# Kernel optimization log

Hardware: AMD Instinct MI355X
Metric: run time of the kernel (lower is better)

The kernel has to match this reference:

```python
import jax, jax.numpy as jnp
import numpy as np

N_NODES = 100000


def gcn_conv(x, W, b, src, dst, num_nodes):
    # PyG GCNConv: h = x @ W; out_i = sum_j norm_ij * h_j + b
    # with self-loops already appended to (src, dst) and
    # norm_ij = deg^{-1/2}[src] * deg^{-1/2}[dst].
    h = x @ W  # [N, out]
    deg = jax.ops.segment_sum(jnp.ones_like(src, dtype=h.dtype), dst, num_segments=num_nodes)
    dinv = jnp.where(deg > 0, jax.lax.rsqrt(deg), 0.0)
    norm = dinv[src] * dinv[dst]  # [E]
    msg = h[src] * norm[:, None]  # [E, out]  (gather + scale)
    out = jax.ops.segment_sum(msg, dst, num_segments=num_nodes)  # scatter-add
    return out + b


def setup_inputs() -> dict:
    key = jax.random.key(0)
    ks = jax.random.split(key, 8)
    x = jax.random.normal(ks[0], (N_NODES, 3), dtype=jnp.float32)
    edge_index = jax.random.randint(ks[1], (2, 3200000), 0, N_NODES, dtype=jnp.int64)

    def glorot(k, fan_in, fan_out):
        s = jnp.sqrt(6.0 / (fan_in + fan_out))
        return jax.random.uniform(k, (fan_in, fan_out), jnp.float32, -s, s)

    W1 = glorot(ks[2], 3, 16)
    b1 = jnp.zeros((16,), jnp.float32)
    W2 = glorot(ks[3], 16, 32)
    b2 = jnp.zeros((32,), jnp.float32)
    W3 = glorot(ks[4], 32, 2)
    b3 = jnp.zeros((2,), jnp.float32)
    return {"x": x, "edge_index": edge_index, "W1": W1, "b1": b1,
            "W2": W2, "b2": b2, "W3": W3, "b3": b3}


def reference(x, edge_index, W1, b1, W2, b2, W3, b3):
    num_nodes = x.shape[0]
    # add self-loops once (GCNConv default add_self_loops=True)
    loops = jnp.arange(num_nodes, dtype=edge_index.dtype)
    src = jnp.concatenate([edge_index[0], loops])
    dst = jnp.concatenate([edge_index[1], loops])

    h = jax.nn.relu(gcn_conv(x, W1, b1, src, dst, num_nodes))
    h = jax.nn.relu(gcn_conv(h, W2, b2, src, dst, num_nodes))
    return gcn_conv(h, W3, b3, src, dst, num_nodes)
```

## Files before the change

kernel.cpp:

```cpp
#include <hip/hip_runtime.h>

static constexpr int NND = 100000;
static constexpr int NED = 3200000;
static constexpr int NB  = (NND + 255) / 256;
static constexpr int NCHUNK = 256;
static constexpr int EPC = NED / NCHUNK;
static constexpr int SCAN_N = NB * NCHUNK;

typedef int int4n __attribute__((ext_vector_type(4)));
typedef _Float16 half4n __attribute__((ext_vector_type(4)));
typedef _Float16 half8n __attribute__((ext_vector_type(8)));


__global__ void k_hist(const int* __restrict__ dst, int* __restrict__ counts) {
    __shared__ int h[NB];
    for (int i = threadIdx.x; i < NB; i += 256) h[i] = 0;
    __syncthreads();
    int c = blockIdx.x;
    const int4n* d4 = reinterpret_cast<const int4n*>(dst + c * EPC);
    for (int i = threadIdx.x; i < EPC / 4; i += 256) {
        int4n v = d4[i];
        atomicAdd(&h[v.x >> 8], 1);
        atomicAdd(&h[v.y >> 8], 1);
        atomicAdd(&h[v.z >> 8], 1);
        atomicAdd(&h[v.w >> 8], 1);
    }
    __syncthreads();
    for (int b = threadIdx.x; b < NB; b += 256)
        counts[b * NCHUNK + c] = h[b];
}


__global__ void k_scan1(const int* __restrict__ in, int* __restrict__ excl,
                        int* __restrict__ blockSums, int n) {
    __shared__ int lds[256];
    int tid = threadIdx.x;
    int base = blockIdx.x * 1024 + tid * 4;
    int v[4]; int sum = 0;
#pragma unroll
    for (int k = 0; k < 4; ++k) { int idx = base + k; v[k] = (idx < n) ? in[idx] : 0; sum += v[k]; }
    lds[tid] = sum; __syncthreads();
    for (int off = 1; off < 256; off <<= 1) {
        int x = lds[tid];
        int y = (tid >= off) ? lds[tid - off] : 0;
        __syncthreads();
        lds[tid] = x + y;
        __syncthreads();
    }
    int run = lds[tid] - sum;
#pragma unroll
    for (int k = 0; k < 4; ++k) { int idx = base + k; if (idx < n) excl[idx] = run; run += v[k]; }
    if (tid == 0) blockSums[blockIdx.x] = lds[255];
}

__global__ void k_scan2(int* __restrict__ blockSums, int nb) {
    __shared__ int lds[128];
    int tid = threadIdx.x;
    int v = (tid < nb) ? blockSums[tid] : 0;
    lds[tid] = v; __syncthreads();
    for (int off = 1; off < 128; off <<= 1) {
        int x = lds[tid];
        int y = (tid >= off) ? lds[tid - off] : 0;
        __syncthreads();
        lds[tid] = x + y;
        __syncthreads();
    }
    if (tid < nb) blockSums[tid] = lds[tid] - v;
}

__global__ void k_scan3(int* __restrict__ excl, const int* __restrict__ blockSums,
                        int n, int e) {
    int i = blockIdx.x * blockDim.x + threadIdx.x;
    if (i < n) excl[i] += blockSums[i >> 10];
    if (i == n) excl[n] = e;
}


__global__ void k_part(const int* __restrict__ src, const int* __restrict__ dst,
                       const int* __restrict__ excl, int* __restrict__ tmp) {
    __shared__ int cur[NB];
    int c = blockIdx.x;
    for (int b = threadIdx.x; b < NB; b += 256) cur[b] = excl[b * NCHUNK + c];
    __syncthreads();
    const int4n* s4 = reinterpret_cast<const int4n*>(src + c * EPC);
    const int4n* d4 = reinterpret_cast<const int4n*>(dst + c * EPC);
    for (int i = threadIdx.x; i < EPC / 4; i += 256) {
        int4n sv = __builtin_nontemporal_load(&s4[i]);
        int4n dv = __builtin_nontemporal_load(&d4[i]);
        int ss[4] = {sv.x, sv.y, sv.z, sv.w};
        int dd[4] = {dv.x, dv.y, dv.z, dv.w};
#pragma unroll
        for (int k = 0; k < 4; ++k) {
            int b = dd[k] >> 8;
            int pos = atomicAdd(&cur[b], 1);
            tmp[pos] = ss[k] | ((dd[k] & 255) << 20);
        }
    }
}


__global__ void k_bucket(const int* __restrict__ excl, const int* __restrict__ tmp,
                         int* __restrict__ ssrc, int* __restrict__ rowptr,
                         float* __restrict__ dinv, const float* __restrict__ x,
                         float4* __restrict__ t4) {
    __shared__ int cnt[256];
    __shared__ int lds[256];
    int b = blockIdx.x, t = threadIdx.x;
    int start = excl[b * NCHUNK];
    int end   = excl[(b + 1) * NCHUNK];
    cnt[t] = 0;
    __syncthreads();
    for (int i = start + t; i < end; i += 256)
        atomicAdd(&cnt[tmp[i] >> 20], 1);
    __syncthreads();
    int v = cnt[t];
    lds[t] = v; __syncthreads();
    for (int off = 1; off < 256; off <<= 1) {
        int xv = lds[t];
        int y = (t >= off) ? lds[t - off] : 0;
        __syncthreads();
        lds[t] = xv + y;
        __syncthreads();
    }
    int node = b * 256 + t;
    int rp = start + lds[t] - v;
    if (node < NND) {
        rowptr[node] = rp;
        float d = rsqrtf((float)(v + 1));
        dinv[node] = d;
        const float* xr = x + (size_t)node * 3;
        t4[node] = make_float4(xr[0] * d, xr[1] * d, xr[2] * d, 0.f);
    }
    if (b == 0 && t == 0) rowptr[NND] = NED;
    cnt[t] = rp;
    __syncthreads();
    for (int i = start + t; i < end; i += 256) {
        int p = tmp[i];
        int pos = atomicAdd(&cnt[p >> 20], 1);
        ssrc[pos] = p & 0xFFFFF;
    }
}


__global__ void k_g4mm1(const int* __restrict__ rowptr, const int* __restrict__ ssrc,
                        const float4* __restrict__ t4, const float* __restrict__ dinv,
                        const float* __restrict__ W1, const float* __restrict__ b1,
                        _Float16* __restrict__ t16, int n) {
    __shared__ float sW[48];
    __shared__ float sb[16];
    if (threadIdx.x < 48) sW[threadIdx.x] = W1[threadIdx.x];
    if (threadIdx.x < 16) sb[threadIdx.x] = b1[threadIdx.x];
    __syncthreads();
    int node = blockIdx.x * blockDim.x + threadIdx.x;
    if (node >= n) return;

    float4 a = t4[node];
    float a0 = a.x, a1 = a.y, a2 = a.z;
    int beg = rowptr[node], end = rowptr[node + 1];
    constexpr int U = 8;
    int j = beg;
    for (; j + U <= end; j += U) {
        int s[U];
#pragma unroll
        for (int k = 0; k < U; ++k) s[k] = ssrc[j + k];
        float4 v[U];
#pragma unroll
        for (int k = 0; k < U; ++k) v[k] = t4[s[k]];
#pragma unroll
        for (int k = 0; k < U; ++k) { a0 += v[k].x; a1 += v[k].y; a2 += v[k].z; }
    }
    for (; j < end; ++j) {
        float4 v = t4[ssrc[j]];
        a0 += v.x; a1 += v.y; a2 += v.z;
    }
    float d = dinv[node];
    float p0 = a0 * d, p1 = a1 * d, p2 = a2 * d;
    _Float16* orow = t16 + (size_t)node * 16;
#pragma unroll
    for (int q = 0; q < 2; ++q) {
        half8n o;
#pragma unroll
        for (int r = 0; r < 8; ++r) {
            int jj = q * 8 + r;
            float h = fmaf(p0, sW[jj], fmaf(p1, sW[16 + jj], fmaf(p2, sW[32 + jj], sb[jj])));
            o[r] = (_Float16)(fmaxf(h, 0.f) * d);
        }
        *reinterpret_cast<half8n*>(orow + q * 8) = o;
    }
}


__global__ void k_g16mm(const int* __restrict__ rowptr, const int* __restrict__ ssrc,
                        const _Float16* __restrict__ t16, const float* __restrict__ dinv,
                        const float* __restrict__ W2, const float* __restrict__ b2,
                        const float* __restrict__ W3, float2* __restrict__ t3, int n) {
    __shared__ float sW2[512];
    __shared__ float sb2[32];
    __shared__ float sW3[64];
    for (int i = threadIdx.x; i < 512; i += 256) sW2[i] = W2[i];
    if (threadIdx.x < 32) sb2[threadIdx.x] = b2[threadIdx.x];
    if (threadIdx.x < 64) sW3[threadIdx.x] = W3[threadIdx.x];
    __syncthreads();

    constexpr int U = 8;
    int i = blockIdx.x * blockDim.x + threadIdx.x;
    int node = i >> 2;
    int fv = i & 3;
    if (node >= n) return;
    int f0 = fv * 4;

    float acc0, acc1, acc2, acc3;
    {
        half4n v = *reinterpret_cast<const half4n*>(t16 + (size_t)node * 16 + f0);
        acc0 = (float)v.x; acc1 = (float)v.y; acc2 = (float)v.z; acc3 = (float)v.w;
    }
    int beg = rowptr[node], end = rowptr[node + 1];
    int j = beg;
    for (; j + U <= end; j += U) {
        int s[U];
#pragma unroll
        for (int k = 0; k < U; ++k) s[k] = ssrc[j + k];
        half4n v[U];
#pragma unroll
        for (int k = 0; k < U; ++k)
            v[k] = *reinterpret_cast<const half4n*>(t16 + (size_t)s[k] * 16 + f0);
#pragma unroll
        for (int k = 0; k < U; ++k) {
            acc0 += (float)v[k].x; acc1 += (float)v[k].y;
            acc2 += (float)v[k].z; acc3 += (float)v[k].w;
        }
    }
    for (; j < end; ++j) {
        half4n v = *reinterpret_cast<const half4n*>(t16 + (size_t)ssrc[j] * 16 + f0);
        acc0 += (float)v.x; acc1 += (float)v.y; acc2 += (float)v.z; acc3 += (float)v.w;
    }
    float d = dinv[node];
    float q[4] = {acc0 * d, acc1 * d, acc2 * d, acc3 * d};

    float p1[4], p2[4], p3[4];
#pragma unroll
    for (int c = 0; c < 4; ++c) p1[c] = __shfl_xor(q[c], 1);
#pragma unroll
    for (int c = 0; c < 4; ++c) { p2[c] = __shfl_xor(q[c], 2); p3[c] = __shfl_xor(p1[c], 2); }

    float uu[16];
#pragma unroll
    for (int c = 0; c < 4; ++c) {
        uu[0 + c]  = fv == 0 ? q[c] : fv == 1 ? p1[c] : fv == 2 ? p2[c] : p3[c];
        uu[4 + c]  = fv == 1 ? q[c] : fv == 0 ? p1[c] : fv == 3 ? p2[c] : p3[c];
        uu[8 + c]  = fv == 2 ? q[c] : fv == 3 ? p1[c] : fv == 0 ? p2[c] : p3[c];
        uu[12 + c] = fv == 3 ? q[c] : fv == 2 ? p1[c] : fv == 1 ? p2[c] : p3[c];
    }

    float t30 = 0.f, t31 = 0.f;
    int jbase = fv * 8;
#pragma unroll
    for (int r = 0; r < 8; ++r) {
        int jj = jbase + r;
        float h = sb2[jj];
#pragma unroll
        for (int k = 0; k < 16; ++k) h = fmaf(uu[k], sW2[k * 32 + jj], h);
        h = fmaxf(h, 0.f);
        t30 = fmaf(h, sW3[jj * 2 + 0], t30);
        t31 = fmaf(h, sW3[jj * 2 + 1], t31);
    }
    t30 += __shfl_xor(t30, 1); t30 += __shfl_xor(t30, 2);
    t31 += __shfl_xor(t31, 1); t31 += __shfl_xor(t31, 2);
    if (fv == 0) t3[node] = make_float2(t30 * d, t31 * d);
}


__global__ void k_g2(const int* __restrict__ rowptr, const int* __restrict__ ssrc,
                     const float2* __restrict__ t3, const float* __restrict__ dinv,
                     const float* __restrict__ b3, float2* __restrict__ out, int n) {
    constexpr int U = 8;
    int node = blockIdx.x * blockDim.x + threadIdx.x;
    if (node >= n) return;
    float2 t = t3[node];
    float a0 = t.x, a1 = t.y;
    int beg = rowptr[node], end = rowptr[node + 1];
    int j = beg;
    for (; j + U <= end; j += U) {
        int s[U];
#pragma unroll
        for (int k = 0; k < U; ++k) s[k] = ssrc[j + k];
        float2 v[U];
#pragma unroll
        for (int k = 0; k < U; ++k) v[k] = t3[s[k]];
#pragma unroll
        for (int k = 0; k < U; ++k) { a0 += v[k].x; a1 += v[k].y; }
    }
    for (; j < end; ++j) {
        float2 v = t3[ssrc[j]];
        a0 += v.x; a1 += v.y;
    }
    float d = dinv[node];
    out[node] = make_float2(fmaf(d, a0, b3[0]), fmaf(d, a1, b3[1]));
}


static inline size_t align256(size_t x) { return (x + 255) & ~(size_t)255; }

extern "C" void kernel_launch(void* const* d_in, const int* in_sizes, int n_in,
                              void* d_out, int out_size, void* d_ws, size_t ws_size,
                              hipStream_t stream) {
    const float* x  = (const float*)d_in[0];
    const int*   ei = (const int*)d_in[1];
    const float* W1 = (const float*)d_in[2];
    const float* b1 = (const float*)d_in[3];
    const float* W2 = (const float*)d_in[4];
    const float* b2 = (const float*)d_in[5];
    const float* W3 = (const float*)d_in[6];
    const float* b3 = (const float*)d_in[7];
    float2* out = (float2*)d_out;

    const int* src = ei;
    const int* dst = ei + NED;

    char* p = (char*)d_ws;
    float* dinv   = (float*)p; p += align256(sizeof(float) * (size_t)NND);
    int*   rowptr = (int*)p;   p += align256(sizeof(int) * (size_t)(NND + 1));
    int*   excl   = (int*)p;   p += align256(sizeof(int) * (size_t)(SCAN_N + 1));
    int*   bsums  = (int*)p;   p += align256(sizeof(int) * 128);
    int*   ssrc   = (int*)p;   p += align256(sizeof(int) * (size_t)NED);
    float4* t4    = (float4*)p; p += align256(sizeof(float4) * (size_t)NND);
    float2* t3    = (float2*)p; p += align256(sizeof(float2) * (size_t)NND);
    char*  q      = p;         p += align256(sizeof(int) * (size_t)NED);
    int*   tmp    = (int*)q;
    _Float16* t16 = (_Float16*)q;

    const int B = 256;
    const int gridN = (NND + B - 1) / B;
    const int grid4N = (NND * 4 + B - 1) / B;
    const int nScanBlocks = (SCAN_N + 1023) / 1024;

    k_hist<<<NCHUNK, B, 0, stream>>>(dst, excl);
    k_scan1<<<nScanBlocks, 256, 0, stream>>>(excl, excl, bsums, SCAN_N);
    k_scan2<<<1, 128, 0, stream>>>(bsums, nScanBlocks);
    k_scan3<<<(SCAN_N + 1 + B - 1) / B, B, 0, stream>>>(excl, bsums, SCAN_N, NED);
    k_part<<<NCHUNK, B, 0, stream>>>(src, dst, excl, tmp);
    k_bucket<<<NB, B, 0, stream>>>(excl, tmp, ssrc, rowptr, dinv, x, t4);

    k_g4mm1<<<gridN, B, 0, stream>>>(rowptr, ssrc, t4, dinv, W1, b1, t16, NND);

    k_g16mm<<<grid4N, B, 0, stream>>>(rowptr, ssrc, t16, dinv, W2, b2, W3, t3, NND);

    k_g2<<<gridN, B, 0, stream>>>(rowptr, ssrc, t3, dinv, b3, out, NND);
}
```

Before: 153.3 us.

## Fold scan fixup into consumers, store layer-1 features in fp16, two lanes per node

Removes the k_scan3 kernel: k_part and k_bucket now add the block-sum offsets themselves when reading the exclusive scan, and the final bucket end is fixed to the edge count. The scaled input features t4 are stored as half4 instead of float4, halving the bytes fetched per edge in the first aggregation. The layer-2 kernel assigns two lanes per node with 8-wide fp16 loads instead of four lanes with 4-wide loads, cutting shuffle work and thread count at the cost of more registers per thread. The fp16 input storage adds some rounding error.

```diff
diff --git a/kernel.cpp b/kernel.cpp
--- a/kernel.cpp
+++ b/kernel.cpp
@@ -68,19 +68,16 @@
     if (tid < nb) blockSums[tid] = lds[tid] - v;
 }
 
-__global__ void k_scan3(int* __restrict__ excl, const int* __restrict__ blockSums,
-                        int n, int e) {
-    int i = blockIdx.x * blockDim.x + threadIdx.x;
-    if (i < n) excl[i] += blockSums[i >> 10];
-    if (i == n) excl[n] = e;
-}
-
 
 __global__ void k_part(const int* __restrict__ src, const int* __restrict__ dst,
-                       const int* __restrict__ excl, int* __restrict__ tmp) {
+                       const int* __restrict__ excl, const int* __restrict__ bsums,
+                       int* __restrict__ tmp) {
     __shared__ int cur[NB];
     int c = blockIdx.x;
-    for (int b = threadIdx.x; b < NB; b += 256) cur[b] = excl[b * NCHUNK + c];
+    for (int b = threadIdx.x; b < NB; b += 256) {
+        int i = b * NCHUNK + c;
+        cur[b] = excl[i] + bsums[i >> 10];
+    }
     __syncthreads();
     const int4n* s4 = reinterpret_cast<const int4n*>(src + c * EPC);
     const int4n* d4 = reinterpret_cast<const int4n*>(dst + c * EPC);
@@ -99,15 +96,19 @@
 }
 
 
-__global__ void k_bucket(const int* __restrict__ excl, const int* __restrict__ tmp,
+__global__ void k_bucket(const int* __restrict__ excl, const int* __restrict__ bsums,
+                         const int* __restrict__ tmp,
                          int* __restrict__ ssrc, int* __restrict__ rowptr,
                          float* __restrict__ dinv, const float* __restrict__ x,
-                         float4* __restrict__ t4) {
+                         half4n* __restrict__ t4) {
     __shared__ int cnt[256];
     __shared__ int lds[256];
     int b = blockIdx.x, t = threadIdx.x;
-    int start = excl[b * NCHUNK];
-    int end   = excl[(b + 1) * NCHUNK];
+    int i0 = b * NCHUNK;
+    int start = excl[i0] + bsums[i0 >> 10];
+    int end;
+    if (b == NB - 1) end = NED;
+    else { int i1 = (b + 1) * NCHUNK; end = excl[i1] + bsums[i1 >> 10]; }
     cnt[t] = 0;
     __syncthreads();
     for (int i = start + t; i < end; i += 256)
@@ -129,7 +130,10 @@
         float d = rsqrtf((float)(v + 1));
         dinv[node] = d;
         const float* xr = x + (size_t)node * 3;
-        t4[node] = make_float4(xr[0] * d, xr[1] * d, xr[2] * d, 0.f);
+        half4n o;
+        o.x = (_Float16)(xr[0] * d); o.y = (_Float16)(xr[1] * d);
+        o.z = (_Float16)(xr[2] * d); o.w = (_Float16)0.f;
+        t4[node] = o;
     }
     if (b == 0 && t == 0) rowptr[NND] = NED;
     cnt[t] = rp;
@@ -143,7 +147,7 @@
 
 
 __global__ void k_g4mm1(const int* __restrict__ rowptr, const int* __restrict__ ssrc,
-                        const float4* __restrict__ t4, const float* __restrict__ dinv,
+                        const half4n* __restrict__ t4, const float* __restrict__ dinv,
                         const float* __restrict__ W1, const float* __restrict__ b1,
                         _Float16* __restrict__ t16, int n) {
     __shared__ float sW[48];
@@ -154,8 +158,11 @@
     int node = blockIdx.x * blockDim.x + threadIdx.x;
     if (node >= n) return;
 
-    float4 a = t4[node];
-    float a0 = a.x, a1 = a.y, a2 = a.z;
+    float a0, a1, a2;
+    {
+        half4n a = t4[node];
+        a0 = (float)a.x; a1 = (float)a.y; a2 = (float)a.z;
+    }
     int beg = rowptr[node], end = rowptr[node + 1];
     constexpr int U = 8;
     int j = beg;
@@ -163,15 +170,17 @@
         int s[U];
 #pragma unroll
         for (int k = 0; k < U; ++k) s[k] = ssrc[j + k];
-        float4 v[U];
+        half4n v[U];
 #pragma unroll
         for (int k = 0; k < U; ++k) v[k] = t4[s[k]];
 #pragma unroll
-        for (int k = 0; k < U; ++k) { a0 += v[k].x; a1 += v[k].y; a2 += v[k].z; }
+        for (int k = 0; k < U; ++k) {
+            a0 += (float)v[k].x; a1 += (float)v[k].y; a2 += (float)v[k].z;
+        }
     }
     for (; j < end; ++j) {
-        float4 v = t4[ssrc[j]];
-        a0 += v.x; a1 += v.y; a2 += v.z;
+        half4n v = t4[ssrc[j]];
+        a0 += (float)v.x; a1 += (float)v.y; a2 += (float)v.z;
     }
     float d = dinv[node];
     float p0 = a0 * d, p1 = a1 * d, p2 = a2 * d;
@@ -204,15 +213,16 @@
 
     constexpr int U = 8;
     int i = blockIdx.x * blockDim.x + threadIdx.x;
-    int node = i >> 2;
-    int fv = i & 3;
+    int node = i >> 1;
+    int half = i & 1;
     if (node >= n) return;
-    int f0 = fv * 4;
-
-    float acc0, acc1, acc2, acc3;
+    int f0 = half * 8;
+
+    float acc[8];
     {
-        half4n v = *reinterpret_cast<const half4n*>(t16 + (size_t)node * 16 + f0);
-        acc0 = (float)v.x; acc1 = (float)v.y; acc2 = (float)v.z; acc3 = (float)v.w;
+        half8n v = *reinterpret_cast<const half8n*>(t16 + (size_t)node * 16 + f0);
+#pragma unroll
+        for (int c = 0; c < 8; ++c) acc[c] = (float)v[c];
     }
     int beg = rowptr[node], end = rowptr[node + 1];
     int j = beg;
@@ -220,42 +230,41 @@
         int s[U];
 #pragma unroll
         for (int k = 0; k < U; ++k) s[k] = ssrc[j + k];
-        half4n v[U];
+        half8n v[U];
 #pragma unroll
         for (int k = 0; k < U; ++k)
-            v[k] = *reinterpret_cast<const half4n*>(t16 + (size_t)s[k] * 16 + f0);
+            v[k] = *reinterpret_cast<const half8n*>(t16 + (size_t)s[k] * 16 + f0);
 #pragma unroll
         for (int k = 0; k < U; ++k) {
-            acc0 += (float)v[k].x; acc1 += (float)v[k].y;
-            acc2 += (float)v[k].z; acc3 += (float)v[k].w;
+#pragma unroll
+            for (int c = 0; c < 8; ++c) acc[c] += (float)v[k][c];
         }
     }
     for (; j < end; ++j) {
-        half4n v = *reinterpret_cast<const half4n*>(t16 + (size_t)ssrc[j] * 16 + f0);
-        acc0 += (float)v.x; acc1 += (float)v.y; acc2 += (float)v.z; acc3 += (float)v.w;
+        half8n v = *reinterpret_cast<const half8n*>(t16 + (size_t)ssrc[j] * 16 + f0);
+#pragma unroll
+        for (int c = 0; c < 8; ++c) acc[c] += (float)v[c];
     }
     float d = dinv[node];
-    float q[4] = {acc0 * d, acc1 * d, acc2 * d, acc3 * d};
-
-    float p1[4], p2[4], p3[4];
-#pragma unroll
-    for (int c = 0; c < 4; ++c) p1[c] = __shfl_xor(q[c], 1);
-#pragma unroll
-    for (int c = 0; c < 4; ++c) { p2[c] = __shfl_xor(q[c], 2); p3[c] = __shfl_xor(p1[c], 2); }
+    float q[8];
+#pragma unroll
+    for (int c = 0; c < 8; ++c) q[c] = acc[c] * d;
+
+    float pq[8];
+#pragma unroll
+    for (int c = 0; c < 8; ++c) pq[c] = __shfl_xor(q[c], 1);
 
     float uu[16];
 #pragma unroll
-    for (int c = 0; c < 4; ++c) {
-        uu[0 + c]  = fv == 0 ? q[c] : fv == 1 ? p1[c] : fv == 2 ? p2[c] : p3[c];
-        uu[4 + c]  = fv == 1 ? q[c] : fv == 0 ? p1[c] : fv == 3 ? p2[c] : p3[c];
-        uu[8 + c]  = fv == 2 ? q[c] : fv == 3 ? p1[c] : fv == 0 ? p2[c] : p3[c];
-        uu[12 + c] = fv == 3 ? q[c] : fv == 2 ? p1[c] : fv == 1 ? p2[c] : p3[c];
+    for (int c = 0; c < 8; ++c) {
+        uu[c]     = half ? pq[c] : q[c];
+        uu[8 + c] = half ? q[c]  : pq[c];
     }
 
     float t30 = 0.f, t31 = 0.f;
-    int jbase = fv * 8;
-#pragma unroll
-    for (int r = 0; r < 8; ++r) {
+    int jbase = half * 16;
+#pragma unroll
+    for (int r = 0; r < 16; ++r) {
         int jj = jbase + r;
         float h = sb2[jj];
 #pragma unroll
@@ -264,9 +273,9 @@
         t30 = fmaf(h, sW3[jj * 2 + 0], t30);
         t31 = fmaf(h, sW3[jj * 2 + 1], t31);
     }
-    t30 += __shfl_xor(t30, 1); t30 += __shfl_xor(t30, 2);
-    t31 += __shfl_xor(t31, 1); t31 += __shfl_xor(t31, 2);
-    if (fv == 0) t3[node] = make_float2(t30 * d, t31 * d);
+    t30 += __shfl_xor(t30, 1);
+    t31 += __shfl_xor(t31, 1);
+    if (half == 0) t3[node] = make_float2(t30 * d, t31 * d);
 }
 
 
@@ -323,7 +332,7 @@
     int*   excl   = (int*)p;   p += align256(sizeof(int) * (size_t)(SCAN_N + 1));
     int*   bsums  = (int*)p;   p += align256(sizeof(int) * 128);
     int*   ssrc   = (int*)p;   p += align256(sizeof(int) * (size_t)NED);
-    float4* t4    = (float4*)p; p += align256(sizeof(float4) * (size_t)NND);
+    half4n* t4    = (half4n*)p; p += align256(sizeof(half4n) * (size_t)NND);
     float2* t3    = (float2*)p; p += align256(sizeof(float2) * (size_t)NND);
     char*  q      = p;         p += align256(sizeof(int) * (size_t)NED);
     int*   tmp    = (int*)q;
@@ -331,19 +340,18 @@
 
     const int B = 256;
     const int gridN = (NND + B - 1) / B;
-    const int grid4N = (NND * 4 + B - 1) / B;
+    const int grid2N = (NND * 2 + B - 1) / B;
     const int nScanBlocks = (SCAN_N + 1023) / 1024;
 
     k_hist<<<NCHUNK, B, 0, stream>>>(dst, excl);
     k_scan1<<<nScanBlocks, 256, 0, stream>>>(excl, excl, bsums, SCAN_N);
     k_scan2<<<1, 128, 0, stream>>>(bsums, nScanBlocks);
-    k_scan3<<<(SCAN_N + 1 + B - 1) / B, B, 0, stream>>>(excl, bsums, SCAN_N, NED);
-    k_part<<<NCHUNK, B, 0, stream>>>(src, dst, excl, tmp);
-    k_bucket<<<NB, B, 0, stream>>>(excl, tmp, ssrc, rowptr, dinv, x, t4);
+    k_part<<<NCHUNK, B, 0, stream>>>(src, dst, excl, bsums, tmp);
+    k_bucket<<<NB, B, 0, stream>>>(excl, bsums, tmp, ssrc, rowptr, dinv, x, t4);
 
     k_g4mm1<<<gridN, B, 0, stream>>>(rowptr, ssrc, t4, dinv, W1, b1, t16, NND);
 
-    k_g16mm<<<grid4N, B, 0, stream>>>(rowptr, ssrc, t16, dinv, W2, b2, W3, t3, NND);
+    k_g16mm<<<grid2N, B, 0, stream>>>(rowptr, ssrc, t16, dinv, W2, b2, W3, t3, NND);
 
     k_g2<<<gridN, B, 0, stream>>>(rowptr, ssrc, t3, dinv, b3, out, NND);
 }
```

After: 154.4 us. About the same (+0.7%).
